# Performance work log

Hardware: AMD Instinct MI355X
Metric: run time of the kernel (lower is better)

The kernel has to match this reference:

```python
import jax, jax.numpy as jnp
import numpy as np

N_NODES = 100000
N_EDGES = 1600000
IN_DIM = 128
HEADS = 8
HEAD_DIM = 16  # output_dim 128 / heads 8
NEG_SLOPE = 0.2  # PyG GATConv default LeakyReLU slope


def setup_inputs() -> dict:
    key = jax.random.key(0)
    k1, k2, k3, k4, k5 = jax.random.split(key, 5)
    x = jax.random.normal(k1, (N_NODES, IN_DIM), dtype=jnp.float32)
    edge_index = jax.random.randint(k2, (2, N_EDGES), 0, N_NODES, dtype=jnp.int64)
    scale = 1.0 / np.sqrt(IN_DIM)
    W = jax.random.normal(k3, (IN_DIM, HEADS * HEAD_DIM), dtype=jnp.float32) * scale
    a_src = jax.random.normal(k4, (HEADS, HEAD_DIM), dtype=jnp.float32) * scale
    a_dst = jax.random.normal(k5, (HEADS, HEAD_DIM), dtype=jnp.float32) * scale
    bias = jnp.zeros((HEADS * HEAD_DIM,), dtype=jnp.float32)
    return {"x": x, "edge_index": edge_index, "W": W, "a_src": a_src, "a_dst": a_dst, "bias": bias}


def reference(x, edge_index, W, a_src, a_dst, bias):
    N = x.shape[0]
    H, D = a_src.shape
    # add self-loops (PyG GATConv default add_self_loops=True)
    loop = jnp.arange(N, dtype=edge_index.dtype)
    src = jnp.concatenate([edge_index[0], loop])  # message sources j
    dst = jnp.concatenate([edge_index[1], loop])  # message targets i

    h = (x @ W).reshape(N, H, D)  # per-head projected features
    alpha_src = jnp.sum(h * a_src, axis=-1)  # [N, H]
    alpha_dst = jnp.sum(h * a_dst, axis=-1)  # [N, H]

    # edge-wise attention logits, softmax over incoming edges of each dst node
    e = jax.nn.leaky_relu(alpha_src[src] + alpha_dst[dst], NEG_SLOPE)  # [E', H]
    e_max = jax.ops.segment_max(e, dst, num_segments=N)
    e_exp = jnp.exp(e - e_max[dst])
    denom = jax.ops.segment_sum(e_exp, dst, num_segments=N)
    alpha = e_exp / (denom[dst] + 1e-16)  # [E', H]

    # weighted scatter-sum of source features
    out = jax.ops.segment_sum(alpha[:, :, None] * h[src], dst, num_segments=N)  # [N, H, D]
    out = out.reshape(N, H * D) + bias
    # wrapper: ReLU (concat=True), dropout is identity in eval mode
    return jax.nn.relu(out)
```

## Files before the change

kernel.cpp:

```cpp
#include <hip/hip_runtime.h>
#include <hip/hip_bf16.h>

#define NEG_SLOPE 0.2f
#define NBUCK 782
#define ABLK 8192
#define CAP 3072

typedef __attribute__((ext_vector_type(8))) short bf16x8v;
typedef __attribute__((ext_vector_type(4))) float f32x4;

__device__ __forceinline__ unsigned f2bf_bits(float f) {
    unsigned u = __float_as_uint(f);
    return (u + 0x7fffu + ((u >> 16) & 1u)) >> 16;
}
__device__ __forceinline__ float bflo(unsigned u) { return __uint_as_float(u << 16); }
__device__ __forceinline__ float bfhi(unsigned u) { return __uint_as_float(u & 0xffff0000u); }

__global__ __launch_bounds__(256) void prep_w(const float* __restrict__ W,
                                              short* __restrict__ WtG) {
    int id = blockIdx.x * 256 + threadIdx.x;
    int n = id >> 7, k = id & 127;
    WtG[id] = (short)f2bf_bits(W[k * 128 + n]);
}

__global__ __launch_bounds__(256) void gemm_mfma(const float* __restrict__ x,
                                                 const short* __restrict__ WtG,
                                                 const float* __restrict__ a_src,
                                                 const float* __restrict__ a_dst,
                                                 short* __restrict__ hout,
                                                 float* __restrict__ as,
                                                 float* __restrict__ ad, int N) {
    __shared__ short xs[64 * 136];
    __shared__ short wt[128 * 136];
    const int tid = threadIdx.x;
    const int r0 = blockIdx.x * 64;

#pragma unroll
    for (int p = 0; p < 8; ++p) {
        int idx = p * 256 + tid;
        int n = idx >> 4, kk = (idx & 15) * 8;
        *(uint4*)&wt[n * 136 + kk] = *(const uint4*)(WtG + n * 128 + kk);
    }
#pragma unroll
    for (int p = 0; p < 8; ++p) {
        int lin = p * 1024 + tid * 4;
        int row = lin >> 7, k = lin & 127;
        int gr = r0 + row;
        int grc = gr < N ? gr : N - 1;
        float4 v = *(const float4*)(x + (size_t)grc * 128 + k);
        unsigned p0 = f2bf_bits(v.x) | (f2bf_bits(v.y) << 16);
        unsigned p1 = f2bf_bits(v.z) | (f2bf_bits(v.w) << 16);
        *(uint2*)&xs[row * 136 + k] = make_uint2(p0, p1);
    }
    __syncthreads();

    const int wv = tid >> 6;
    const int lane = tid & 63;
    const int lc = lane & 15, quad = lane >> 4;
    f32x4 acc[8];
#pragma unroll
    for (int c = 0; c < 8; ++c) acc[c] = (f32x4){0.f, 0.f, 0.f, 0.f};
    const short* aB = &xs[(wv * 16 + lc) * 136 + quad * 8];
    const short* bB = &wt[lc * 136 + quad * 8];
#pragma unroll
    for (int kc = 0; kc < 4; ++kc) {
        bf16x8v af = *(const bf16x8v*)(aB + kc * 32);
#pragma unroll
        for (int c = 0; c < 8; ++c) {
            bf16x8v bf = *(const bf16x8v*)(bB + c * (16 * 136) + kc * 32);
            acc[c] = __builtin_amdgcn_mfma_f32_16x16x32_bf16(af, bf, acc[c], 0, 0, 0);
        }
    }

    const int rowb = r0 + wv * 16 + quad * 4;
#pragma unroll
    for (int c = 0; c < 8; ++c) {
        float asc = a_src[c * 16 + lc];
        float adc = a_dst[c * 16 + lc];
        float sv[4], dv[4];
#pragma unroll
        for (int r = 0; r < 4; ++r) {
            float hv = acc[c][r];
            int row = rowb + r;
            if (row < N) hout[(size_t)row * 128 + c * 16 + lc] = (short)f2bf_bits(hv);
            sv[r] = hv * asc;
            dv[r] = hv * adc;
        }
#pragma unroll
        for (int m = 1; m <= 8; m <<= 1) {
#pragma unroll
            for (int r = 0; r < 4; ++r) {
                sv[r] += __shfl_xor(sv[r], m);
                dv[r] += __shfl_xor(dv[r], m);
            }
        }
        if (lc == 0) {
#pragma unroll
            for (int r = 0; r < 4; ++r) {
                int row = rowb + r;
                if (row < N) { as[row * 8 + c] = sv[r]; ad[row * 8 + c] = dv[r]; }
            }
        }
    }
}

__global__ __launch_bounds__(1024) void bucket_edges(const int* __restrict__ ei, int E,
                                                     unsigned* __restrict__ slab,
                                                     int* __restrict__ cntG,
                                                     int* __restrict__ startG) {
    __shared__ int hist[1024];
    __shared__ int cur[NBUCK];
    __shared__ int wpart[16];
    const int t = threadIdx.x;
    const int blk = blockIdx.x;
    const int base = blk * ABLK;
    int count = E - base; if (count > ABLK) count = ABLK;

    int sr[8], dr[8];
    hist[t] = 0;
#pragma unroll
    for (int k = 0; k < 8; ++k) {
        int i = k * 1024 + t;
        if (i < count) { sr[k] = ei[base + i]; dr[k] = ei[E + base + i]; }
    }
    __syncthreads();
#pragma unroll
    for (int k = 0; k < 8; ++k) {
        int i = k * 1024 + t;
        if (i < count) atomicAdd(&hist[dr[k] >> 7], 1);
    }
    __syncthreads();
    int v = hist[t];
    int lane = t & 63, wid = t >> 6;
    int sc = v;
#pragma unroll
    for (int off = 1; off < 64; off <<= 1) { int u = __shfl_up(sc, off); if (lane >= off) sc += u; }
    if (lane == 63) wpart[wid] = sc;
    __syncthreads();
    if (wid == 0 && lane < 16) {
        int wv = wpart[lane], wsum = wv;
#pragma unroll
        for (int off = 1; off < 16; off <<= 1) { int u = __shfl_up(wsum, off); if (lane >= off) wsum += u; }
        wpart[lane] = wsum - wv;
    }
    __syncthreads();
    int excl = sc - v + wpart[wid];
    if (t < NBUCK) {
        cntG[blk * NBUCK + t]   = v;
        startG[blk * NBUCK + t] = excl;
        cur[t] = excl;
    }
    __syncthreads();
#pragma unroll
    for (int k = 0; k < 8; ++k) {
        int i = k * 1024 + t;
        if (i < count) {
            int d = dr[k];
            int pos = atomicAdd(&cur[d >> 7], 1);
            slab[(size_t)blk * ABLK + pos] = (unsigned)sr[k] | ((unsigned)(d & 127) << 17);
        }
    }
}

__global__ __launch_bounds__(512) void build_csr(const unsigned* __restrict__ slab,
                                                 const int* __restrict__ cntG,
                                                 const int* __restrict__ startG,
                                                 int nblk, int N,
                                                 int* __restrict__ rowS,
                                                 int* __restrict__ rowE,
                                                 int* __restrict__ sortedSrc) {
    __shared__ int eL[CAP];
    __shared__ int incl[512];
    __shared__ int cS[512];
    __shared__ int stS[512];
    __shared__ int lp[128];
    __shared__ int wpart[8];
    __shared__ int halfSum;
    const int bb = blockIdx.x;
    const int t = threadIdx.x;
    const int nodeBase = bb << 7;
    const int bBase = bb * CAP;

    int c = 0, st = 0;
    if (t < nblk) { c = cntG[t * NBUCK + bb]; st = startG[t * NBUCK + bb]; }
    cS[t] = c; stS[t] = st;
    if (t < 128) lp[t] = 0;
    int lane = t & 63, wid = t >> 6;
    int sc = c;
#pragma unroll
    for (int off = 1; off < 64; off <<= 1) { int u = __shfl_up(sc, off); if (lane >= off) sc += u; }
    if (lane == 63) wpart[wid] = sc;
    __syncthreads();
    if (wid == 0 && lane < 8) {
        int wv = wpart[lane], wsum = wv;
#pragma unroll
        for (int off = 1; off < 8; off <<= 1) { int u = __shfl_up(wsum, off); if (lane >= off) wsum += u; }
        wpart[lane] = wsum - wv;
    }
    __syncthreads();
    incl[t] = sc + wpart[wid];
    __syncthreads();
    int total = incl[511];
    if (total > CAP) total = CAP;
    for (int e = t; e < total; e += 512) {
        int lo = 0, hi = nblk - 1;
        while (lo < hi) { int mid = (lo + hi) >> 1; if (incl[mid] > e) hi = mid; else lo = mid + 1; }
        int loc = e - (incl[lo] - cS[lo]);
        eL[e] = (int)slab[(size_t)lo * ABLK + stS[lo] + loc];
    }
    __syncthreads();
    for (int e = t; e < total; e += 512) atomicAdd(&lp[((unsigned)eL[e]) >> 17], 1);
    __syncthreads();
    int cnt = 0, s2 = 0;
    if (t < 128) {
        cnt = lp[t];
        s2 = cnt;
#pragma unroll
        for (int off = 1; off < 64; off <<= 1) { int u = __shfl_up(s2, off); if (lane >= off) s2 += u; }
        if (t == 63) halfSum = s2;
    }
    __syncthreads();
    if (t < 128) {
        int inc2 = s2 + (t >= 64 ? halfSum : 0);
        int ex = inc2 - cnt;
        int gn = nodeBase + t;
        if (gn < N) { rowS[gn] = bBase + ex; rowE[gn] = bBase + ex + cnt; }
        lp[t] = ex;
    }
    __syncthreads();
    for (int e = t; e < total; e += 512) {
        unsigned pk = (unsigned)eL[e];
        int pos = atomicAdd(&lp[pk >> 17], 1);
        sortedSrc[bBase + pos] = (int)(pk & 0x1FFFFu);
    }
}

__global__ __launch_bounds__(256) void aggregate(const int* __restrict__ rowS,
                                                 const int* __restrict__ rowE,
                                                 const int* __restrict__ sortedSrc,
                                                 const short* __restrict__ h,
                                                 const float* __restrict__ as,
                                                 const float* __restrict__ ad,
                                                 const float* __restrict__ bias,
                                                 float* __restrict__ out, int N) {
    int node = blockIdx.x * 4 + (threadIdx.x >> 6);
    if (node >= N) return;
    int lane = threadIdx.x & 63;
    int g = lane >> 4, p = lane & 15, hh = p >> 1;
    int start = rowS[node], end = rowE[node];
    float adv = ad[node * 8 + hh];

    float acc[8];
#pragma unroll
    for (int k = 0; k < 8; ++k) acc[k] = 0.f;
    float dsum = 0.f;

    int e = start + g;
    float asv = 0.f; uint4 hr;
    if (e < end) {
        int j = sortedSrc[e];
        asv = as[j * 8 + hh];
        hr = *(const uint4*)(h + (size_t)j * 128 + p * 8);
    }
    while (e < end) {
        int en = e + 4;
        float asn = 0.f; uint4 hn;
        if (en < end) {
            int jn = sortedSrc[en];
            asn = as[jn * 8 + hh];
            hn = *(const uint4*)(h + (size_t)jn * 128 + p * 8);
        }
        float tt = asv + adv;
        tt = tt > 0.f ? tt : NEG_SLOPE * tt;
        float w = __expf(tt);
        acc[0] += w * bflo(hr.x); acc[1] += w * bfhi(hr.x);
        acc[2] += w * bflo(hr.y); acc[3] += w * bfhi(hr.y);
        acc[4] += w * bflo(hr.z); acc[5] += w * bfhi(hr.z);
        acc[6] += w * bflo(hr.w); acc[7] += w * bfhi(hr.w);
        dsum += w;
        asv = asn; hr = hn; e = en;
    }
#pragma unroll
    for (int m = 16; m <= 32; m <<= 1) {
#pragma unroll
        for (int k = 0; k < 8; ++k) acc[k] += __shfl_xor(acc[k], m);
        dsum += __shfl_xor(dsum, m);
    }
    {
        float tt = as[node * 8 + hh] + adv;
        tt = tt > 0.f ? tt : NEG_SLOPE * tt;
        float w = __expf(tt);
        uint4 hv = *(const uint4*)(h + (size_t)node * 128 + p * 8);
        acc[0] += w * bflo(hv.x); acc[1] += w * bfhi(hv.x);
        acc[2] += w * bflo(hv.y); acc[3] += w * bfhi(hv.y);
        acc[4] += w * bflo(hv.z); acc[5] += w * bfhi(hv.z);
        acc[6] += w * bflo(hv.w); acc[7] += w * bfhi(hv.w);
        dsum += w;
    }
    float inv = 1.0f / (dsum + 1e-16f);
    float4 b0 = *(const float4*)(bias + p * 8);
    float4 b1 = *(const float4*)(bias + p * 8 + 4);
    float o0 = acc[0] * inv + b0.x, o1 = acc[1] * inv + b0.y;
    float o2 = acc[2] * inv + b0.z, o3 = acc[3] * inv + b0.w;
    float o4 = acc[4] * inv + b1.x, o5 = acc[5] * inv + b1.y;
    float o6 = acc[6] * inv + b1.z, o7 = acc[7] * inv + b1.w;
    o0 = o0 > 0.f ? o0 : 0.f; o1 = o1 > 0.f ? o1 : 0.f;
    o2 = o2 > 0.f ? o2 : 0.f; o3 = o3 > 0.f ? o3 : 0.f;
    o4 = o4 > 0.f ? o4 : 0.f; o5 = o5 > 0.f ? o5 : 0.f;
    o6 = o6 > 0.f ? o6 : 0.f; o7 = o7 > 0.f ? o7 : 0.f;
    *(float4*)(out + (size_t)node * 128 + p * 8)     = make_float4(o0, o1, o2, o3);
    *(float4*)(out + (size_t)node * 128 + p * 8 + 4) = make_float4(o4, o5, o6, o7);
}

extern "C" void kernel_launch(void* const* d_in, const int* in_sizes, int n_in,
                              void* d_out, int out_size, void* d_ws, size_t ws_size,
                              hipStream_t stream) {
    const float* x     = (const float*)d_in[0];
    const int*   ei    = (const int*)d_in[1];
    const float* W     = (const float*)d_in[2];
    const float* a_src = (const float*)d_in[3];
    const float* a_dst = (const float*)d_in[4];
    const float* bias  = (const float*)d_in[5];
    float* out = (float*)d_out;

    const int N = in_sizes[0] / 128;
    const int E = in_sizes[1] / 2;
    const int nblk = (E + ABLK - 1) / ABLK;

    char* ws = (char*)d_ws;
    size_t off = 0;
    auto alloc = [&](size_t bytes) { void* p = ws + off; off = (off + bytes + 255) & ~(size_t)255; return p; };
    short*    h         = (short*)alloc((size_t)N * 128 * 2);
    float*    as        = (float*)alloc((size_t)N * 8 * 4);
    float*    ad        = (float*)alloc((size_t)N * 8 * 4);
    unsigned* slab      = (unsigned*)alloc((size_t)nblk * ABLK * 4);
    int*      cntG      = (int*)alloc((size_t)nblk * NBUCK * 4);
    int*      startG    = (int*)alloc((size_t)nblk * NBUCK * 4);
    int*      sortedSrc = (int*)alloc((size_t)NBUCK * CAP * 4);
    int*      rowS      = (int*)alloc((size_t)N * 4);
    int*      rowE      = (int*)alloc((size_t)N * 4);
    short*    WtG       = (short*)alloc((size_t)128 * 128 * 2);

    prep_w<<<64, 256, 0, stream>>>(W, WtG);
    gemm_mfma<<<(N + 63) / 64, 256, 0, stream>>>(x, WtG, a_src, a_dst, h, as, ad, N);
    bucket_edges<<<nblk, 1024, 0, stream>>>(ei, E, slab, cntG, startG);
    build_csr<<<NBUCK, 512, 0, stream>>>(slab, cntG, startG, nblk, N, rowS, rowE, sortedSrc);
    aggregate<<<(N + 3) / 4, 256, 0, stream>>>(rowS, rowE, sortedSrc, h, as, ad, bias, out, N);
}
```

Before: 246.5 us.

## Fold attention vectors into GEMM, restructure CSR gather and aggregate lane mapping

Precomputes W·a_src and W·a_dst as 16 extra bf16 columns of the weight matrix, so the GEMM produces the attention logits directly through one more MFMA tile and drops the shuffle reductions. build_csr now copies each slab segment contiguously per wavefront instead of binary-searching per edge. The aggregate kernel now gives each lane one full head (16 features) and processes 8 edges in parallel per wave instead of 4. The trade-offs are bf16 rounding of the folded logit weights, more registers in aggregate, and a wider cross-lane reduction.

```diff
diff --git a/kernel.cpp b/kernel.cpp
--- a/kernel.cpp
+++ b/kernel.cpp
@@ -17,29 +17,44 @@
 __device__ __forceinline__ float bfhi(unsigned u) { return __uint_as_float(u & 0xffff0000u); }
 
 __global__ __launch_bounds__(256) void prep_w(const float* __restrict__ W,
-                                              short* __restrict__ WtG) {
+                                              const float* __restrict__ a_src,
+                                              const float* __restrict__ a_dst,
+                                              short* __restrict__ WtE) {
     int id = blockIdx.x * 256 + threadIdx.x;
+    if (id >= 144 * 128) return;
     int n = id >> 7, k = id & 127;
-    WtG[id] = (short)f2bf_bits(W[k * 128 + n]);
+    float v;
+    if (n < 128) {
+        v = W[k * 128 + n];
+    } else if (n < 136) {
+        int hh = n - 128; float s = 0.f;
+#pragma unroll
+        for (int d = 0; d < 16; ++d) s += W[k * 128 + hh * 16 + d] * a_src[hh * 16 + d];
+        v = s;
+    } else {
+        int hh = n - 136; float s = 0.f;
+#pragma unroll
+        for (int d = 0; d < 16; ++d) s += W[k * 128 + hh * 16 + d] * a_dst[hh * 16 + d];
+        v = s;
+    }
+    WtE[id] = (short)f2bf_bits(v);
 }
 
 __global__ __launch_bounds__(256) void gemm_mfma(const float* __restrict__ x,
-                                                 const short* __restrict__ WtG,
-                                                 const float* __restrict__ a_src,
-                                                 const float* __restrict__ a_dst,
+                                                 const short* __restrict__ WtE,
                                                  short* __restrict__ hout,
                                                  float* __restrict__ as,
                                                  float* __restrict__ ad, int N) {
     __shared__ short xs[64 * 136];
-    __shared__ short wt[128 * 136];
+    __shared__ short wt[144 * 136];
     const int tid = threadIdx.x;
     const int r0 = blockIdx.x * 64;
 
 #pragma unroll
-    for (int p = 0; p < 8; ++p) {
+    for (int p = 0; p < 9; ++p) {
         int idx = p * 256 + tid;
         int n = idx >> 4, kk = (idx & 15) * 8;
-        *(uint4*)&wt[n * 136 + kk] = *(const uint4*)(WtG + n * 128 + kk);
+        *(uint4*)&wt[n * 136 + kk] = *(const uint4*)(WtE + n * 128 + kk);
     }
 #pragma unroll
     for (int p = 0; p < 8; ++p) {
@@ -57,16 +72,16 @@
     const int wv = tid >> 6;
     const int lane = tid & 63;
     const int lc = lane & 15, quad = lane >> 4;
-    f32x4 acc[8];
-#pragma unroll
-    for (int c = 0; c < 8; ++c) acc[c] = (f32x4){0.f, 0.f, 0.f, 0.f};
+    f32x4 acc[9];
+#pragma unroll
+    for (int c = 0; c < 9; ++c) acc[c] = (f32x4){0.f, 0.f, 0.f, 0.f};
     const short* aB = &xs[(wv * 16 + lc) * 136 + quad * 8];
     const short* bB = &wt[lc * 136 + quad * 8];
 #pragma unroll
     for (int kc = 0; kc < 4; ++kc) {
         bf16x8v af = *(const bf16x8v*)(aB + kc * 32);
 #pragma unroll
-        for (int c = 0; c < 8; ++c) {
+        for (int c = 0; c < 9; ++c) {
             bf16x8v bf = *(const bf16x8v*)(bB + c * (16 * 136) + kc * 32);
             acc[c] = __builtin_amdgcn_mfma_f32_16x16x32_bf16(af, bf, acc[c], 0, 0, 0);
         }
@@ -75,31 +90,18 @@
     const int rowb = r0 + wv * 16 + quad * 4;
 #pragma unroll
     for (int c = 0; c < 8; ++c) {
-        float asc = a_src[c * 16 + lc];
-        float adc = a_dst[c * 16 + lc];
-        float sv[4], dv[4];
 #pragma unroll
         for (int r = 0; r < 4; ++r) {
-            float hv = acc[c][r];
             int row = rowb + r;
-            if (row < N) hout[(size_t)row * 128 + c * 16 + lc] = (short)f2bf_bits(hv);
-            sv[r] = hv * asc;
-            dv[r] = hv * adc;
-        }
-#pragma unroll
-        for (int m = 1; m <= 8; m <<= 1) {
-#pragma unroll
-            for (int r = 0; r < 4; ++r) {
-                sv[r] += __shfl_xor(sv[r], m);
-                dv[r] += __shfl_xor(dv[r], m);
-            }
-        }
-        if (lc == 0) {
-#pragma unroll
-            for (int r = 0; r < 4; ++r) {
-                int row = rowb + r;
-                if (row < N) { as[row * 8 + c] = sv[r]; ad[row * 8 + c] = dv[r]; }
-            }
+            if (row < N) hout[(size_t)row * 128 + c * 16 + lc] = (short)f2bf_bits(acc[c][r]);
+        }
+    }
+#pragma unroll
+    for (int r = 0; r < 4; ++r) {
+        int row = rowb + r;
+        if (row < N) {
+            if (lc < 8) as[row * 8 + lc] = acc[8][r];
+            else        ad[row * 8 + (lc - 8)] = acc[8][r];
         }
     }
 }
@@ -202,11 +204,11 @@
     __syncthreads();
     int total = incl[511];
     if (total > CAP) total = CAP;
-    for (int e = t; e < total; e += 512) {
-        int lo = 0, hi = nblk - 1;
-        while (lo < hi) { int mid = (lo + hi) >> 1; if (incl[mid] > e) hi = mid; else lo = mid + 1; }
-        int loc = e - (incl[lo] - cS[lo]);
-        eL[e] = (int)slab[(size_t)lo * ABLK + stS[lo] + loc];
+    for (int s = wid; s < nblk; s += 8) {
+        int cc = cS[s];
+        int off0 = incl[s] - cc;
+        const unsigned* p = slab + (size_t)s * ABLK + stS[s];
+        for (int i = lane; i < cc; i += 64) eL[off0 + i] = (int)p[i];
     }
     __syncthreads();
     for (int e = t; e < total; e += 512) atomicAdd(&lp[((unsigned)eL[e]) >> 17], 1);
@@ -246,70 +248,84 @@
     int node = blockIdx.x * 4 + (threadIdx.x >> 6);
     if (node >= N) return;
     int lane = threadIdx.x & 63;
-    int g = lane >> 4, p = lane & 15, hh = p >> 1;
+    int g = lane >> 3, p = lane & 7;
     int start = rowS[node], end = rowE[node];
-    float adv = ad[node * 8 + hh];
-
-    float acc[8];
-#pragma unroll
-    for (int k = 0; k < 8; ++k) acc[k] = 0.f;
+    float adv = ad[node * 8 + p];
+
+    float acc[16];
+#pragma unroll
+    for (int k = 0; k < 16; ++k) acc[k] = 0.f;
     float dsum = 0.f;
 
     int e = start + g;
-    float asv = 0.f; uint4 hr;
+    float asv = 0.f; uint4 h0, h1;
     if (e < end) {
         int j = sortedSrc[e];
-        asv = as[j * 8 + hh];
-        hr = *(const uint4*)(h + (size_t)j * 128 + p * 8);
+        asv = as[j * 8 + p];
+        const uint4* hp = (const uint4*)(h + (size_t)j * 128 + p * 16);
+        h0 = hp[0]; h1 = hp[1];
     }
     while (e < end) {
-        int en = e + 4;
-        float asn = 0.f; uint4 hn;
+        int en = e + 8;
+        float asn = 0.f; uint4 n0, n1;
         if (en < end) {
             int jn = sortedSrc[en];
-            asn = as[jn * 8 + hh];
-            hn = *(const uint4*)(h + (size_t)jn * 128 + p * 8);
+            asn = as[jn * 8 + p];
+            const uint4* hp = (const uint4*)(h + (size_t)jn * 128 + p * 16);
+            n0 = hp[0]; n1 = hp[1];
         }
         float tt = asv + adv;
         tt = tt > 0.f ? tt : NEG_SLOPE * tt;
         float w = __expf(tt);
-        acc[0] += w * bflo(hr.x); acc[1] += w * bfhi(hr.x);
-        acc[2] += w * bflo(hr.y); acc[3] += w * bfhi(hr.y);
-        acc[4] += w * bflo(hr.z); acc[5] += w * bfhi(hr.z);
-        acc[6] += w * bflo(hr.w); acc[7] += w * bfhi(hr.w);
+        acc[0]  += w * bflo(h0.x); acc[1]  += w * bfhi(h0.x);
+        acc[2]  += w * bflo(h0.y); acc[3]  += w * bfhi(h0.y);
+        acc[4]  += w * bflo(h0.z); acc[5]  += w * bfhi(h0.z);
+        acc[6]  += w * bflo(h0.w); acc[7]  += w * bfhi(h0.w);
+        acc[8]  += w * bflo(h1.x); acc[9]  += w * bfhi(h1.x);
+        acc[10] += w * bflo(h1.y); acc[11] += w * bfhi(h1.y);
+        acc[12] += w * bflo(h1.z); acc[13] += w * bfhi(h1.z);
+        acc[14] += w * bflo(h1.w); acc[15] += w * bfhi(h1.w);
         dsum += w;
-        asv = asn; hr = hn; e = en;
-    }
-#pragma unroll
-    for (int m = 16; m <= 32; m <<= 1) {
-#pragma unroll
-        for (int k = 0; k < 8; ++k) acc[k] += __shfl_xor(acc[k], m);
+        asv = asn; h0 = n0; h1 = n1; e = en;
+    }
+#pragma unroll
+    for (int m = 8; m <= 32; m <<= 1) {
+#pragma unroll
+        for (int k = 0; k < 16; ++k) acc[k] += __shfl_xor(acc[k], m);
         dsum += __shfl_xor(dsum, m);
     }
     {
-        float tt = as[node * 8 + hh] + adv;
+        float tt = as[node * 8 + p] + adv;
         tt = tt > 0.f ? tt : NEG_SLOPE * tt;
         float w = __expf(tt);
-        uint4 hv = *(const uint4*)(h + (size_t)node * 128 + p * 8);
-        acc[0] += w * bflo(hv.x); acc[1] += w * bfhi(hv.x);
-        acc[2] += w * bflo(hv.y); acc[3] += w * bfhi(hv.y);
-        acc[4] += w * bflo(hv.z); acc[5] += w * bfhi(hv.z);
-        acc[6] += w * bflo(hv.w); acc[7] += w * bfhi(hv.w);
+        const uint4* hp = (const uint4*)(h + (size_t)node * 128 + p * 16);
+        uint4 s0 = hp[0], s1 = hp[1];
+        acc[0]  += w * bflo(s0.x); acc[1]  += w * bfhi(s0.x);
+        acc[2]  += w * bflo(s0.y); acc[3]  += w * bfhi(s0.y);
+        acc[4]  += w * bflo(s0.z); acc[5]  += w * bfhi(s0.z);
+        acc[6]  += w * bflo(s0.w); acc[7]  += w * bfhi(s0.w);
+        acc[8]  += w * bflo(s1.x); acc[9]  += w * bfhi(s1.x);
+        acc[10] += w * bflo(s1.y); acc[11] += w * bfhi(s1.y);
+        acc[12] += w * bflo(s1.z); acc[13] += w * bfhi(s1.z);
+        acc[14] += w * bflo(s1.w); acc[15] += w * bfhi(s1.w);
         dsum += w;
     }
-    float inv = 1.0f / (dsum + 1e-16f);
-    float4 b0 = *(const float4*)(bias + p * 8);
-    float4 b1 = *(const float4*)(bias + p * 8 + 4);
-    float o0 = acc[0] * inv + b0.x, o1 = acc[1] * inv + b0.y;
-    float o2 = acc[2] * inv + b0.z, o3 = acc[3] * inv + b0.w;
-    float o4 = acc[4] * inv + b1.x, o5 = acc[5] * inv + b1.y;
-    float o6 = acc[6] * inv + b1.z, o7 = acc[7] * inv + b1.w;
-    o0 = o0 > 0.f ? o0 : 0.f; o1 = o1 > 0.f ? o1 : 0.f;
-    o2 = o2 > 0.f ? o2 : 0.f; o3 = o3 > 0.f ? o3 : 0.f;
-    o4 = o4 > 0.f ? o4 : 0.f; o5 = o5 > 0.f ? o5 : 0.f;
-    o6 = o6 > 0.f ? o6 : 0.f; o7 = o7 > 0.f ? o7 : 0.f;
-    *(float4*)(out + (size_t)node * 128 + p * 8)     = make_float4(o0, o1, o2, o3);
-    *(float4*)(out + (size_t)node * 128 + p * 8 + 4) = make_float4(o4, o5, o6, o7);
+    if (g == 0) {
+        float inv = 1.0f / (dsum + 1e-16f);
+        float* op = out + (size_t)node * 128 + p * 16;
+        const float* bp = bias + p * 16;
+#pragma unroll
+        for (int q = 0; q < 4; ++q) {
+            float4 bv = *(const float4*)(bp + q * 4);
+            float o0 = acc[q * 4 + 0] * inv + bv.x;
+            float o1 = acc[q * 4 + 1] * inv + bv.y;
+            float o2 = acc[q * 4 + 2] * inv + bv.z;
+            float o3 = acc[q * 4 + 3] * inv + bv.w;
+            o0 = o0 > 0.f ? o0 : 0.f; o1 = o1 > 0.f ? o1 : 0.f;
+            o2 = o2 > 0.f ? o2 : 0.f; o3 = o3 > 0.f ? o3 : 0.f;
+            *(float4*)(op + q * 4) = make_float4(o0, o1, o2, o3);
+        }
+    }
 }
 
 extern "C" void kernel_launch(void* const* d_in, const int* in_sizes, int n_in,
@@ -339,10 +355,10 @@
     int*      sortedSrc = (int*)alloc((size_t)NBUCK * CAP * 4);
     int*      rowS      = (int*)alloc((size_t)N * 4);
     int*      rowE      = (int*)alloc((size_t)N * 4);
-    short*    WtG       = (short*)alloc((size_t)128 * 128 * 2);
-
-    prep_w<<<64, 256, 0, stream>>>(W, WtG);
-    gemm_mfma<<<(N + 63) / 64, 256, 0, stream>>>(x, WtG, a_src, a_dst, h, as, ad, N);
+    short*    WtE       = (short*)alloc((size_t)144 * 128 * 2);
+
+    prep_w<<<72, 256, 0, stream>>>(W, a_src, a_dst, WtE);
+    gemm_mfma<<<(N + 63) / 64, 256, 0, stream>>>(x, WtE, h, as, ad, N);
     bucket_edges<<<nblk, 1024, 0, stream>>>(ei, E, slab, cntG, startG);
     build_csr<<<NBUCK, 512, 0, stream>>>(slab, cntG, startG, nblk, N, rowS, rowE, sortedSrc);
     aggregate<<<(N + 3) / 4, 256, 0, stream>>>(rowS, rowE, sortedSrc, h, as, ad, bias, out, N);
```

After: 235.0 us. 1.05x faster.
